# Performance work log

Measured on AMD Instinct MI355X. Metric: run time of the kernel, lower is better.

## Reference

```python
import jax, jax.numpy as jnp
import numpy as np

PS = 10            # patchsize
ADJ = PS // 2      # use_adj offset (patches centered on query pixel)
K = 7              # neighbors
WS = 29            # search window
R = WS // 2
SCALE = 1.0        # dist_scale


def setup_inputs() -> dict:
    key = jax.random.key(0)
    k1, k2, k3 = jax.random.split(key, 3)
    x = jax.random.normal(k1, (1, 16, 96, 96), jnp.float32)
    xe = jax.random.normal(k2, (1, 8, 96, 96), jnp.float32)
    ye = jax.random.normal(k3, (1, 8, 96, 96), jnp.float32)
    return {"x": x, "xe": xe, "ye": ye}


def _patch_pad(img):
    # zero border for patch reads (dnls iUnfold border='zero', adj=ps//2)
    return jnp.pad(img, ((0, 0), (ADJ, PS - 1 - ADJ), (ADJ, PS - 1 - ADJ)))


def _boxsum(a, h, w):
    # sum over ps x ps windows via integral image; a: (h+PS-1, w+PS-1) -> (h, w)
    c = jnp.pad(jnp.cumsum(jnp.cumsum(a, 0), 1), ((1, 0), (1, 0)))
    return c[PS:PS + h, PS:PS + w] - c[:h, PS:PS + w] - c[PS:PS + h, :w] + c[:h, :w]


def _extract_patches(imgp, h, w):
    # imgp: (C, h+PS-1, w+PS-1) patch-padded -> (h*w, C*PS*PS)
    rows = jnp.arange(h)[:, None] + jnp.arange(PS)[None, :]
    cols = jnp.arange(w)[:, None] + jnp.arange(PS)[None, :]
    pat = imgp[:, rows][:, :, :, cols]          # (C, h, PS, w, PS)
    return pat.transpose(1, 3, 0, 2, 4).reshape(h * w, -1)


def _forward(x, xe, ye):
    x, xe, ye = x[0], xe[0], ye[0]              # t = 1
    pad1 = lambda a: jnp.pad(a, ((0, 0), (1, 1), (1, 1)))  # F.pad(.., (1,1,1,1))
    x, xe, ye = pad1(x), pad1(xe), pad1(ye)
    y = x                                        # y=None -> y=x path
    c, h, w = x.shape
    H2, W2 = h + PS - 1, w + PS - 1

    # ---- L2 patch search over WS x WS displacement window ----
    yep = _patch_pad(ye)
    xep = _patch_pad(xe)
    xebig = jnp.pad(xep, ((0, 0), (R, R), (R, R)))
    disp = jnp.arange(WS * WS)
    dys = disp // WS - R
    dxs = disp % WS - R

    def dist_for(dy, dx):
        xs = jax.lax.dynamic_slice(xebig, (0, R + dy, R + dx), (xep.shape[0], H2, W2))
        sq = jnp.sum((yep - xs) ** 2, axis=0)   # (H2, W2)
        return _boxsum(sq, h, w)                # (h, w)

    dists = jax.vmap(dist_for)(dys, dxs)        # (WS*WS, h, w)

    # invalidate out-of-bounds centers + self (remove_self=True)
    ni = jnp.arange(h)[None, :, None] + dys[:, None, None]
    nj = jnp.arange(w)[None, None, :] + dxs[:, None, None]
    valid = (ni >= 0) & (ni < h) & (nj >= 0) & (nj < w) & \
            ((dys != 0) | (dxs != 0))[:, None, None]
    dists = jnp.where(valid, dists, jnp.float32(1e10))

    dq = dists.reshape(WS * WS, h * w).T        # (Q, WS*WS)
    neg, idx = jax.lax.top_k(-dq, K)            # k smallest dists; neg = -l2
    Wgt = jax.nn.softmax(SCALE * neg, axis=-1)  # softmax(scale * (-dists))

    # absolute flat neighbor indices
    qi = jnp.arange(h * w) // w
    qj = jnp.arange(h * w) % w
    flat = (qi[:, None] + dys[idx]) * w + (qj[:, None] + dxs[idx])  # (Q, K)

    # ---- indexed weighted aggregation of x patches ----
    xp = _extract_patches(_patch_pad(x), h, w)  # (Q, c*PS*PS)
    z_patches = jnp.einsum('qk,qkc->qc', Wgt, xp[flat])

    # ---- fold with overlap count (iFoldz: vid / zvid) ----
    zp = z_patches.reshape(h, w, c, PS, PS).transpose(2, 0, 1, 3, 4)
    vid = jnp.zeros((c, H2, W2), x.dtype)
    for oy in range(PS):
        for ox in range(PS):
            vid = vid.at[:, oy:oy + h, ox:ox + w].add(zp[:, :, :, oy, ox])
    ra, ca = jnp.arange(H2), jnp.arange(W2)
    cnt_r = (jnp.minimum(ra, h - 1) - jnp.maximum(ra - PS + 1, 0) + 1).astype(x.dtype)
    cnt_c = (jnp.minimum(ca, w - 1) - jnp.maximum(ca - PS + 1, 0) + 1).astype(x.dtype)
    zvid = cnt_r[:, None] * cnt_c[None, :]
    z = vid[:, ADJ:ADJ + h, ADJ:ADJ + w] / zvid[ADJ:ADJ + h, ADJ:ADJ + w][None]

    z = z - y
    out = jnp.concatenate([y, z], axis=0)       # (2c, h, w)
    return out[None, :, 1:-1, 1:-1]             # crop the border pad


def reference(x, xe, ye):
    return _forward(x, xe, ye)
```

## Files before the change

### kernel.cpp

```cpp
#include <hip/hip_runtime.h>

#define PS   10
#define KNN  7
#define WSZ  29
#define RR   14
#define IH   96
#define IW   96
#define CH   16
#define CE   8
#define HH   98
#define QN   (HH*HH)
#define ND   (WSZ*WSZ)
#define XTW  124
#define XTP  14
#define YEW  107
#define YEH  112
#define XEW  144
#define XEH  140
#define QP   9800

#define OFF_SV   8241856ull
#define OFF_SD   (OFF_SV + 76832ull)
#define OFF_CV   (OFF_SD + 76832ull)
#define OFF_CI   (OFF_CV + 307328ull)
#define OFF_XT   (OFF_CI + 307328ull)
#define OFF_YEP  (OFF_XT + 246016ull)
#define OFF_XEP  (OFF_YEP + 95872ull)

__device__ __forceinline__ int imin(int a, int b){ return a<b?a:b; }
__device__ __forceinline__ int imax(int a, int b){ return a>b?a:b; }

__global__ __launch_bounds__(256) void k_prep(const float* __restrict__ x,
                                              const float* __restrict__ xe,
                                              const float* __restrict__ ye,
                                              float* __restrict__ xT,
                                              float* __restrict__ xeP,
                                              float* __restrict__ yeP) {
    int t = blockIdx.x*256 + threadIdx.x;
    if (t < XTW*XTW) {
        int u = t / XTW, v = t % XTW;
        int ui = u - XTP, vi = v - XTP;
        bool inb = ((unsigned)ui < (unsigned)IH) && ((unsigned)vi < (unsigned)IW);
        int off = inb ? (ui*IW + vi) : 0;
        float4* dst = (float4*)(xT + (size_t)t*CH);
        #pragma unroll
        for (int c4 = 0; c4 < 4; ++c4) {
            float4 val;
            val.x = inb ? x[(c4*4+0)*IH*IW + off] : 0.f;
            val.y = inb ? x[(c4*4+1)*IH*IW + off] : 0.f;
            val.z = inb ? x[(c4*4+2)*IH*IW + off] : 0.f;
            val.w = inb ? x[(c4*4+3)*IH*IW + off] : 0.f;
            dst[c4] = val;
        }
        return;
    }
    t -= XTW*XTW;
    if (t < YEH*YEW) {
        int i = t / YEW, j = t % YEW;
        bool inb = ((unsigned)(i-6) < (unsigned)IH) && ((unsigned)(j-6) < (unsigned)IW);
        int off = inb ? ((i-6)*IW + (j-6)) : 0;
        float4* dst = (float4*)(yeP + (size_t)t*CE);
        #pragma unroll
        for (int c4 = 0; c4 < 2; ++c4) {
            float4 val;
            val.x = inb ? ye[(c4*4+0)*IH*IW + off] : 0.f;
            val.y = inb ? ye[(c4*4+1)*IH*IW + off] : 0.f;
            val.z = inb ? ye[(c4*4+2)*IH*IW + off] : 0.f;
            val.w = inb ? ye[(c4*4+3)*IH*IW + off] : 0.f;
            dst[c4] = val;
        }
        return;
    }
    t -= YEH*YEW;
    if (t < XEH*XEW) {
        int i = t / XEW, j = t % XEW;
        bool inb = ((unsigned)(i-20) < (unsigned)IH) && ((unsigned)(j-20) < (unsigned)IW);
        int off = inb ? ((i-20)*IW + (j-20)) : 0;
        float4* dst = (float4*)(xeP + (size_t)t*CE);
        #pragma unroll
        for (int c4 = 0; c4 < 2; ++c4) {
            float4 val;
            val.x = inb ? xe[(c4*4+0)*IH*IW + off] : 0.f;
            val.y = inb ? xe[(c4*4+1)*IH*IW + off] : 0.f;
            val.z = inb ? xe[(c4*4+2)*IH*IW + off] : 0.f;
            val.w = inb ? xe[(c4*4+3)*IH*IW + off] : 0.f;
            dst[c4] = val;
        }
    }
}

__global__ __launch_bounds__(128, 4) void k_dist(const float* __restrict__ xeP,
                                                 const float* __restrict__ yeP,
                                                 float* __restrict__ dist) {
    __shared__ float ring[3][544];

    int b     = blockIdx.x;
    int dx_i  = b % 29;
    int rem   = b / 29;
    int strip = rem % 7;
    int dyg   = rem / 7;
    int y0s   = strip * 14;
    int t     = threadIdx.x;
    int tc    = t < 107 ? t : 106;
    int csw   = tc + (tc >> 2);
    bool wact = t < 107;

    int dyi_u = t / 25;
    int cg_u  = t - dyi_u*25;
    int dy_u  = dyg*4 + dyi_u - 14;
    bool plane_ok = (t < 100) && (dyg*4 + dyi_u <= 28);
    int dx    = dx_i - 14;
    bool selfd = (dy_u == 0) && (dx == 0);
    int x0u   = 4*cg_u;
    const float* rbp = &ring[0][0] + dyi_u*136 + 5*cg_u;
    float* dout = dist + (size_t)((dyg*4 + dyi_u)*29 + dx_i)*QP + x0u;

    const size_t xstep = (size_t)XEW*CE, ystep = (size_t)YEW*CE;
    const float* xload = xeP + ((size_t)(y0s + dyg*4)*XEW + (tc + dx_i))*CE;
    const float* yload = yeP + ((size_t)y0s*YEW + tc)*CE;

    float4 xr[4][2];
    #pragma unroll
    for (int r = 0; r < 3; ++r) {
        xr[r][0] = ((const float4*)xload)[0];
        xr[r][1] = ((const float4*)xload)[1];
        xload += xstep;
    }
    float wsum[4] = {0.f,0.f,0.f,0.f};
    float hist[4][10];

#define DSTEP(S) { \
    float4 xna = ((const float4*)xload)[0]; \
    float4 xnb = ((const float4*)xload)[1]; \
    xload += xstep; \
    float4 ya  = ((const float4*)yload)[0]; \
    float4 yb  = ((const float4*)yload)[1]; \
    yload += ystep; \
    xr[((S)+3)&3][0] = xna; xr[((S)+3)&3][1] = xnb; \
    _Pragma("unroll") \
    for (int dyi = 0; dyi < 4; ++dyi) { \
        float4 xa = xr[((S)+dyi)&3][0]; \
        float4 xb = xr[((S)+dyi)&3][1]; \
        float d0=ya.x-xa.x, d1=ya.y-xa.y, d2=ya.z-xa.z, d3=ya.w-xa.w; \
        float d4=yb.x-xb.x, d5=yb.y-xb.y, d6=yb.z-xb.z, d7=yb.w-xb.w; \
        float a = d0*d0; \
        a=fmaf(d1,d1,a); a=fmaf(d2,d2,a); a=fmaf(d3,d3,a); \
        a=fmaf(d4,d4,a); a=fmaf(d5,d5,a); a=fmaf(d6,d6,a); \
        a=fmaf(d7,d7,a); \
        float w = wsum[dyi] + a; \
        if ((S) >= 10) w -= hist[dyi][(S)%10]; \
        wsum[dyi] = w; \
        hist[dyi][(S)%10] = a; \
        if ((S) >= 9 && wact) ring[(S)%3][dyi*136 + csw] = w; \
    } \
    __syncthreads(); \
    if ((S) >= 9 && plane_ok) { \
        const float* bse = rbp + ((S)%3)*544; \
        float v0=bse[0],v1=bse[1],v2=bse[2],v3=bse[3]; \
        float v5=bse[5],v6=bse[6],v7=bse[7],v8=bse[8]; \
        float v10=bse[10],v11=bse[11],v12=bse[12],v13=bse[13],v15=bse[15]; \
        float s0 = ((v0+v1)+(v2+v3)) + ((v5+v6)+(v7+v8)) + (v10+v11); \
        float s1 = s0 - v0 + v12; \
        float s2 = s1 - v1 + v13; \
        float s3 = s2 - v2 + v15; \
        int y0 = y0s + (S) - 9; \
        int ni = y0 + dy_u; \
        bool okr = ((unsigned)ni < 98u) && !selfd; \
        float4 o; \
        o.x = (okr && (unsigned)(x0u+0+dx) < 98u) ? s0 : 1e10f; \
        o.y = (okr && (unsigned)(x0u+1+dx) < 98u) ? s1 : 1e10f; \
        o.z = (okr && (unsigned)(x0u+2+dx) < 98u) ? s2 : 1e10f; \
        o.w = (okr && (unsigned)(x0u+3+dx) < 98u) ? s3 : 1e10f; \
        *(float4*)(dout + y0*100) = o; \
    } \
}

    DSTEP(0)  DSTEP(1)  DSTEP(2)  DSTEP(3)  DSTEP(4)
    DSTEP(5)  DSTEP(6)  DSTEP(7)  DSTEP(8)  DSTEP(9)
    DSTEP(10) DSTEP(11) DSTEP(12) DSTEP(13) DSTEP(14)
    DSTEP(15) DSTEP(16) DSTEP(17) DSTEP(18) DSTEP(19)
    DSTEP(20) DSTEP(21) DSTEP(22)
#undef DSTEP
}

__global__ __launch_bounds__(256) void k_topkA(const float* __restrict__ dist,
                                               float* __restrict__ cv, int* __restrict__ ci) {
    __shared__ float lv[3*64*8];
    __shared__ int   lix[3*64*8];
    int wv = threadIdx.x >> 6, ln = threadIdx.x & 63;
    int qb = blockIdx.x % 151;
    int rg = blockIdx.x / 151;
    int q  = qb*64 + ln;
    int qq = q < QN ? q : QN-1;
    int y0 = qq / 98, x0 = qq - y0*98;
    int off = y0*100 + x0;

    int rbase = rg*210 + (rg > 0 ? 1 : 0);
    int ndr   = (rg == 0) ? 211 : 210;
    int s0 = rbase + wv*53;
    int s1 = imin(rbase + ndr, s0 + 53);

    float ld[KNN]; int li[KNN];
    #pragma unroll
    for (int k = 0; k < KNN; ++k) { ld[k] = 1e30f; li[k] = -1; }

    auto INS = [&](float v, int dsp) {
        float cvv = v; int cii = dsp;
        #pragma unroll
        for (int k = 0; k < KNN; ++k) {
            bool sw = cvv < ld[k];
            float tf = ld[k]; int ti = li[k];
            ld[k] = sw ? cvv : tf;  li[k] = sw ? cii : ti;
            cvv   = sw ? tf : cvv;  cii   = sw ? ti : cii;
        }
    };

    #pragma unroll 2
    for (int dd = s0; dd < s1; ++dd)
        INS(dist[(size_t)dd*QP + off], dd);

    if (wv) {
        int bse = ((wv-1)*64 + ln)*8;
        #pragma unroll
        for (int r = 0; r < KNN; ++r) { lv[bse+r] = ld[r]; lix[bse+r] = li[r]; }
    }
    __syncthreads();
    if (wv == 0 && q < QN) {
        #pragma unroll
        for (int w = 0; w < 3; ++w) {
            int bse = (w*64 + ln)*8;
            #pragma unroll
            for (int r = 0; r < KNN; ++r) INS(lv[bse+r], lix[bse+r]);
        }
        #pragma unroll
        for (int r = 0; r < KNN; ++r) {
            cv[(q*4 + rg)*8 + r] = ld[r];
            ci[(q*4 + rg)*8 + r] = li[r];
        }
    }
}

__global__ __launch_bounds__(256) void k_topkB(const float* __restrict__ cv,
                                               const int* __restrict__ ci,
                                               float* __restrict__ sv, int* __restrict__ sd) {
    int q = blockIdx.x*256 + threadIdx.x;
    if (q >= QN) return;

    float ld[KNN]; int li[KNN];
    #pragma unroll
    for (int k = 0; k < KNN; ++k) { ld[k] = 1e30f; li[k] = -1; }

    auto INS = [&](float v, int dsp) {
        float cvv = v; int cii = dsp;
        #pragma unroll
        for (int k = 0; k < KNN; ++k) {
            bool sw = cvv < ld[k];
            float tf = ld[k]; int ti = li[k];
            ld[k] = sw ? cvv : tf;  li[k] = sw ? cii : ti;
            cvv   = sw ? tf : cvv;  cii   = sw ? ti : cii;
        }
    };

    #pragma unroll
    for (int rg = 0; rg < 4; ++rg) {
        #pragma unroll
        for (int r = 0; r < KNN; ++r)
            INS(cv[(q*4 + rg)*8 + r], ci[(q*4 + rg)*8 + r]);
    }

    float e[KNN]; float ssum = 0.f;
    #pragma unroll
    for (int r = 0; r < KNN; ++r) { e[r] = __expf(ld[0] - ld[r]); ssum += e[r]; }
    float inv = 1.f / ssum;
    #pragma unroll
    for (int r = 0; r < KNN; ++r) {
        sv[q*8 + r] = e[r] * inv;
        int dsp = li[r];
        int dyk = dsp / WSZ - RR, dxk = dsp % WSZ - RR;
        sd[q*8 + r] = (dyk*XTW + dxk) * CH;
    }
}

__global__ __launch_bounds__(512) void k_agg(const float* __restrict__ xT,
                                             const float* __restrict__ wgt,
                                             const int* __restrict__ dlt,
                                             float* __restrict__ out) {
    __shared__ float2 lw[13*13*7];
    __shared__ float4 red[7*64];
    int tid = threadIdx.x;
    int tb = blockIdx.x;
    int ai0 = (tb / 24) * 4, bi0 = (tb % 24) * 4;

    for (int u = tid; u < 13*13*7; u += 512) {
        int lq = u / 7, k = u - lq*7;
        int lqi = lq / 13, lqj = lq - lqi*13;
        int qi = ai0 - 3 + lqi, qj = bi0 - 3 + lqj;
        bool ok = ((unsigned)qi < 98u) && ((unsigned)qj < 98u);
        int q = ok ? (qi*98 + qj) : 0;
        float w = ok ? wgt[q*8 + k] : 0.f;
        int  dl = ok ? dlt[q*8 + k] : 0;
        lw[u] = make_float2(w, __int_as_float(dl));
    }
    __syncthreads();

    int og   = tid >> 6;
    int rem  = tid & 63;
    int quad = rem & 3;
    int pl   = rem >> 2;
    int py   = pl >> 2, px = pl & 3;
    int ai = ai0 + py, bi = bi0 + px;
    int base = ((ai + XTP)*XTW + (bi + XTP))*CH + quad*4;

    float ax=0.f, ay=0.f, az=0.f, aw=0.f;
    #pragma unroll
    for (int c = 0; c < 13; ++c) {
        int u = og*13 + c;
        if (u >= 100) break;
        int oy = u / 10, ox = u - oy*10;
        int lq = (py + 9 - oy)*13 + (px + 9 - ox);
        const float2* f2p = lw + lq*7;
        #pragma unroll
        for (int k = 0; k < KNN; ++k) {
            float2 wd = f2p[k];
            int dl = __float_as_int(wd.y);
            const float4 xv = *(const float4*)(xT + base + dl);
            ax = fmaf(wd.x, xv.x, ax); ay = fmaf(wd.x, xv.y, ay);
            az = fmaf(wd.x, xv.z, az); aw = fmaf(wd.x, xv.w, aw);
        }
    }

    if (og) {
        float4 pr; pr.x=ax; pr.y=ay; pr.z=az; pr.w=aw;
        red[(og-1)*64 + rem] = pr;
    }
    __syncthreads();
    if (og == 0) {
        #pragma unroll
        for (int w = 0; w < 7; ++w) {
            float4 pr = red[w*64 + rem];
            ax += pr.x; ay += pr.y; az += pr.z; aw += pr.w;
        }
        int i = ai + 6, j = bi + 6;
        float cr = (float)(imin(i, 97) - imax(i - 9, 0) + 1);
        float cc = (float)(imin(j, 97) - imax(j - 9, 0) + 1);
        float inv = 1.f / (cr * cc);
        float4 xs = *(const float4*)(xT + base);
        int p = ai*IW + bi;
        int ch0 = quad*4;
        out[(ch0+0)*IH*IW + p] = xs.x;
        out[(ch0+1)*IH*IW + p] = xs.y;
        out[(ch0+2)*IH*IW + p] = xs.z;
        out[(ch0+3)*IH*IW + p] = xs.w;
        out[(16+ch0+0)*IH*IW + p] = ax*inv - xs.x;
        out[(16+ch0+1)*IH*IW + p] = ay*inv - xs.y;
        out[(16+ch0+2)*IH*IW + p] = az*inv - xs.z;
        out[(16+ch0+3)*IH*IW + p] = aw*inv - xs.w;
    }
}

extern "C" void kernel_launch(void* const* d_in, const int* in_sizes, int n_in,
                              void* d_out, int out_size, void* d_ws, size_t ws_size,
                              hipStream_t stream) {
    const float* x  = (const float*)d_in[0];
    const float* xe = (const float*)d_in[1];
    const float* ye = (const float*)d_in[2];
    float* out = (float*)d_out;
    float* ws  = (float*)d_ws;

    float* dist = ws;
    float* sv   = ws + OFF_SV;
    int*   sd   = (int*)(ws + OFF_SD);
    float* cv   = ws + OFF_CV;
    int*   ci   = (int*)(ws + OFF_CI);
    float* xT   = ws + OFF_XT;
    float* yeP  = ws + OFF_YEP;
    float* xeP  = ws + OFF_XEP;

    {
        int total = XTW*XTW + YEH*YEW + XEH*XEW;
        hipLaunchKernelGGL(k_prep, dim3((total + 255)/256), dim3(256), 0, stream,
                           x, xe, ye, xT, xeP, yeP);
    }
    hipLaunchKernelGGL(k_dist,  dim3(8*29*7), dim3(128), 0, stream, xeP, yeP, dist);
    hipLaunchKernelGGL(k_topkA, dim3(151*4), dim3(256), 0, stream, dist, cv, ci);
    hipLaunchKernelGGL(k_topkB, dim3((QN + 255)/256), dim3(256), 0, stream, cv, ci, sv, sd);
    hipLaunchKernelGGL(k_agg,   dim3(24*24), dim3(512), 0, stream, xT, sv, sd, out);
}
```

Measured before the change: 79.12 us.

## Split k_dist column sums per wavefront to remove block barriers

Each of the two 64-lane wavefronts in k_dist now owns an overlapping column range with its own shared-memory slice. Each wavefront then does the horizontal boxsum from data only it wrote, so the per-row __syncthreads and the 3-deep ring buffer are gone. Each thread now loads its column index directly with no clamp, and the x-row register ring grows from 4 to 5 entries. The cost is some duplicated halo columns, extra registers, and a partial float2 store at the right edge. Correctness now depends on lockstep execution within a wavefront and compiler ordering of the shared-memory accesses without a barrier.

```diff
diff --git a/kernel.cpp b/kernel.cpp
--- a/kernel.cpp
+++ b/kernel.cpp
@@ -92,7 +92,7 @@
 __global__ __launch_bounds__(128, 4) void k_dist(const float* __restrict__ xeP,
                                                  const float* __restrict__ yeP,
                                                  float* __restrict__ dist) {
-    __shared__ float ring[3][544];
+    __shared__ float cs[2][4][72];
 
     int b     = blockIdx.x;
     int dx_i  = b % 29;
@@ -100,28 +100,37 @@
     int strip = rem % 7;
     int dyg   = rem / 7;
     int y0s   = strip * 14;
-    int t     = threadIdx.x;
-    int tc    = t < 107 ? t : 106;
-    int csw   = tc + (tc >> 2);
-    bool wact = t < 107;
-
-    int dyi_u = t / 25;
-    int cg_u  = t - dyi_u*25;
-    int dy_u  = dyg*4 + dyi_u - 14;
-    bool plane_ok = (t < 100) && (dyg*4 + dyi_u <= 28);
+    int tid   = threadIdx.x;
+    int wid   = tid >> 6;
+    int lane  = tid & 63;
+    int col   = wid ? (43 + lane) : lane;
+    int widx  = lane + (wid ? 3 : 0);
+
+    int nun   = wid ? 12 : 13;
+    int dyi_c = imin(lane / nun, 3);
+    int u     = lane - dyi_c * nun;
+    bool cact = lane < nun * 4;
+    int x0u   = wid ? (52 + 4*u) : (4*u);
+    bool full4 = (wid == 0) || (u < 11);
+    const float* rdp = &cs[wid][dyi_c][ wid ? (12 + 4*u) : (4*u) ];
+    int plane = dyg*4 + dyi_c;
+    bool plane_ok = cact && (plane <= 28);
+    int dy_c  = plane - 14;
     int dx    = dx_i - 14;
-    bool selfd = (dy_u == 0) && (dx == 0);
-    int x0u   = 4*cg_u;
-    const float* rbp = &ring[0][0] + dyi_u*136 + 5*cg_u;
-    float* dout = dist + (size_t)((dyg*4 + dyi_u)*29 + dx_i)*QP + x0u;
+    bool selfd = (dy_c == 0) && (dx == 0);
+    bool okx0 = (unsigned)(x0u+0+dx) < 98u;
+    bool okx1 = (unsigned)(x0u+1+dx) < 98u;
+    bool okx2 = (unsigned)(x0u+2+dx) < 98u;
+    bool okx3 = (unsigned)(x0u+3+dx) < 98u;
+    float* dout = dist + (size_t)(imin(plane,28)*29 + dx_i)*QP + x0u;
 
     const size_t xstep = (size_t)XEW*CE, ystep = (size_t)YEW*CE;
-    const float* xload = xeP + ((size_t)(y0s + dyg*4)*XEW + (tc + dx_i))*CE;
-    const float* yload = yeP + ((size_t)y0s*YEW + tc)*CE;
-
-    float4 xr[4][2];
-    #pragma unroll
-    for (int r = 0; r < 3; ++r) {
+    const float* xload = xeP + ((size_t)(y0s + dyg*4)*XEW + (col + dx_i))*CE;
+    const float* yload = yeP + ((size_t)y0s*YEW + col)*CE;
+
+    float4 xr[5][2];
+    #pragma unroll
+    for (int r = 0; r < 4; ++r) {
         xr[r][0] = ((const float4*)xload)[0];
         xr[r][1] = ((const float4*)xload)[1];
         xload += xstep;
@@ -136,11 +145,11 @@
     float4 ya  = ((const float4*)yload)[0]; \
     float4 yb  = ((const float4*)yload)[1]; \
     yload += ystep; \
-    xr[((S)+3)&3][0] = xna; xr[((S)+3)&3][1] = xnb; \
+    xr[(S+4)%5][0] = xna; xr[(S+4)%5][1] = xnb; \
     _Pragma("unroll") \
     for (int dyi = 0; dyi < 4; ++dyi) { \
-        float4 xa = xr[((S)+dyi)&3][0]; \
-        float4 xb = xr[((S)+dyi)&3][1]; \
+        float4 xa = xr[(S+dyi)%5][0]; \
+        float4 xb = xr[(S+dyi)%5][1]; \
         float d0=ya.x-xa.x, d1=ya.y-xa.y, d2=ya.z-xa.z, d3=ya.w-xa.w; \
         float d4=yb.x-xb.x, d5=yb.y-xb.y, d6=yb.z-xb.z, d7=yb.w-xb.w; \
         float a = d0*d0; \
@@ -151,27 +160,25 @@
         if ((S) >= 10) w -= hist[dyi][(S)%10]; \
         wsum[dyi] = w; \
         hist[dyi][(S)%10] = a; \
-        if ((S) >= 9 && wact) ring[(S)%3][dyi*136 + csw] = w; \
+        cs[wid][dyi][widx] = w; \
     } \
-    __syncthreads(); \
     if ((S) >= 9 && plane_ok) { \
-        const float* bse = rbp + ((S)%3)*544; \
-        float v0=bse[0],v1=bse[1],v2=bse[2],v3=bse[3]; \
-        float v5=bse[5],v6=bse[6],v7=bse[7],v8=bse[8]; \
-        float v10=bse[10],v11=bse[11],v12=bse[12],v13=bse[13],v15=bse[15]; \
-        float s0 = ((v0+v1)+(v2+v3)) + ((v5+v6)+(v7+v8)) + (v10+v11); \
-        float s1 = s0 - v0 + v12; \
-        float s2 = s1 - v1 + v13; \
-        float s3 = s2 - v2 + v15; \
+        float v0=rdp[0], v1=rdp[1], v2=rdp[2], v3=rdp[3]; \
+        float v4=rdp[4], v5=rdp[5], v6=rdp[6], v7=rdp[7]; \
+        float v8=rdp[8], v9=rdp[9], v10=rdp[10], v11=rdp[11], v12=rdp[12]; \
+        float s0 = ((v0+v1)+(v2+v3)) + ((v4+v5)+(v6+v7)) + (v8+v9); \
+        float s1 = s0 - v0 + v10; \
+        float s2 = s1 - v1 + v11; \
+        float s3 = s2 - v2 + v12; \
         int y0 = y0s + (S) - 9; \
-        int ni = y0 + dy_u; \
-        bool okr = ((unsigned)ni < 98u) && !selfd; \
+        bool okr = ((unsigned)(y0 + dy_c) < 98u) && !selfd; \
         float4 o; \
-        o.x = (okr && (unsigned)(x0u+0+dx) < 98u) ? s0 : 1e10f; \
-        o.y = (okr && (unsigned)(x0u+1+dx) < 98u) ? s1 : 1e10f; \
-        o.z = (okr && (unsigned)(x0u+2+dx) < 98u) ? s2 : 1e10f; \
-        o.w = (okr && (unsigned)(x0u+3+dx) < 98u) ? s3 : 1e10f; \
-        *(float4*)(dout + y0*100) = o; \
+        o.x = (okr && okx0) ? s0 : 1e10f; \
+        o.y = (okr && okx1) ? s1 : 1e10f; \
+        o.z = (okr && okx2) ? s2 : 1e10f; \
+        o.w = (okr && okx3) ? s3 : 1e10f; \
+        if (full4) *(float4*)(dout + y0*100) = o; \
+        else       *(float2*)(dout + y0*100) = make_float2(o.x, o.y); \
     } \
 }
 
```

New measurement: 78.96 us. No clear change (-0.2%).
